# Kernel optimization log

Measured on AMD Instinct MI355X. Metric: run time of the kernel, lower is better.

## Reference

```python
import jax, jax.numpy as jnp
import numpy as np
from jax import lax

B, D, N, K, POOL = 256, 512, 50000, 32, 1024
ALPHA, BETA, LAMB = 1.0, 1.0, 1e-4
TAU, EPS, DELTA = 0.1, 0.1, 1e-3
SINKHORN_ITERS = 200


def matrix_sqrt(A):
    # differentiable symmetric PSD matrix sqrt via eigendecomposition
    w, v = jnp.linalg.eigh(A)
    w = jnp.clip(w, 0.0)
    return (v * jnp.sqrt(w)) @ v.T


def ridge_cov(M, delta):
    Dm = M.shape[0]
    S = M + (jnp.trace(M) / Dm * delta) * jnp.eye(Dm, dtype=M.dtype)
    return 0.5 * (S + S.T)


def sinkhorn(p, q, C, eps):
    # entropic OT, fixed-iteration Sinkhorn (ot.sinkhorn equivalent)
    Kmat = jnp.exp(-C / eps)
    def step(uv, _):
        u, v = uv
        u = p / (Kmat @ v + 1e-16)
        v = q / (Kmat.T @ u + 1e-16)
        return (u, v), None
    (u, v), _ = lax.scan(step, (jnp.ones_like(p), jnp.ones_like(q)), None, length=SINKHORN_ITERS)
    return u[:, None] * Kmat * v[None, :]


def setup_inputs():
    key = jax.random.key(0)
    k1, k2, k3, k4, k5, k6 = jax.random.split(key, 6)
    return {
        "q_batch": jax.random.normal(k1, (B, D), jnp.float32),
        "q_indices": jax.random.randint(k2, (B,), 0, POOL),
        "W": jax.random.normal(k3, (D, D), jnp.float32) * 0.05,
        "X": jax.random.normal(k4, (N, D), jnp.float32),
        "pre_indices": jax.random.randint(k5, (POOL, K), 0, N),
        "pre_weights": jax.random.uniform(k6, (POOL, K), jnp.float32, 0.1, 1.0),
    }


def _forward(q_batch, W, X, pre_weights, q_indices, pre_indices):
    T = q_batch @ W  # model := single linear layer, T_q_batch [B, D]
    # ---- distribution alignment (2-Wasserstein between Gaussians) ----
    mu_X = X.mean(0)
    Sigma_X = ridge_cov(jnp.cov(X, rowvar=False).astype(X.dtype), DELTA)
    mu_t = T.mean(0)
    Sigma_t = ridge_cov(jnp.cov(T, rowvar=False).astype(T.dtype), max(DELTA, 1e-4))
    term_mean = jnp.sum((mu_t - mu_X) ** 2)
    s_t = matrix_sqrt(Sigma_t)
    M = s_t @ Sigma_X @ s_t
    s_m = matrix_sqrt(0.5 * (M + M.T))
    term_cov = jnp.trace(Sigma_X + Sigma_t - 2.0 * s_m)
    loss_dist = term_mean + jnp.clip(term_cov, 0.0)
    # ---- kNN consistency with entropic OT ----
    T_sg = lax.stop_gradient(T)  # faiss search is on detached queries
    d2 = (T_sg ** 2).sum(1, keepdims=True) - 2.0 * T_sg @ X.T + (X ** 2).sum(1)[None, :]
    _, post_idx = lax.top_k(-d2, K)  # exact brute-force kNN == faiss IndexFlatL2
    Xn = X[post_idx]  # [B, K, D]
    l2 = ((T[:, None, :] - Xn) ** 2).sum(-1)  # [B, K], grads flow through T
    post_w = jax.nn.softmax(-l2 / TAU, axis=1)
    post_w = jnp.clip(post_w, 1e-8)
    post_w = post_w / post_w.sum(1, keepdims=True)
    pre_idx_b = pre_indices[q_indices]  # [B, K]
    pre_w = jnp.clip(pre_weights[q_indices], 1e-8)
    pre_w = pre_w / pre_w.sum(1, keepdims=True)
    # fixed-size support = concat(pre, post) of size 2K; duplicated points cost 0
    # to move between, so OT value matches the deduped-union formulation
    support = jnp.concatenate([pre_idx_b, post_idx], axis=1)  # [B, 2K]
    S = X[support]  # [B, 2K, D]
    sq = (S ** 2).sum(-1)
    C = jnp.clip(sq[:, :, None] + sq[:, None, :] - 2.0 * jnp.einsum('bid,bjd->bij', S, S), 0.0)
    med = jnp.median(C.reshape(C.shape[0], -1), axis=1)
    C = C / (med[:, None, None] + 1e-8)
    zeros = jnp.zeros_like(pre_w)
    p = jnp.concatenate([pre_w, zeros], axis=1)   # pre mass on first K slots
    q = jnp.concatenate([zeros, post_w], axis=1)  # post mass on last K slots
    plans = jax.vmap(lambda pp, qq, cc: sinkhorn(pp, qq, cc, EPS))(p, q, C)
    loss_knn = (plans * C).sum((1, 2)).mean()
    loss_reg = 0.5 * jnp.sum(W ** 2)
    total = ALPHA * loss_dist + BETA * loss_knn + LAMB * loss_reg
    return total, loss_dist, loss_knn


def reference(q_batch, q_indices, W, X, pre_indices, pre_weights):
    return _forward(q_batch, W, X, pre_weights, q_indices, pre_indices)
```

## Files before the change

kernel.cpp:

```cpp
#include <hip/hip_runtime.h>
#include <float.h>
#include <math.h>

#define BB 256
#define DD 512
#define NN 50000
#define KK 32
#define NS_ITERS 11
#define PARTS 8
#define PCH 6250

#define OFF_G     0
#define OFF_SC    262144
#define OFF_CS    262208
#define OFF_CSS   262720
#define ZERO_F    263232
#define OFF_T     263232
#define OFF_TC    394304
#define OFF_P     525376
#define OFF_H     656448
#define OFF_XSQ   723008
#define OFF_RUNI  781200
#define OFF_PW    789392
#define OFF_PRW   797584
// ... 151 lines not shown
  }
  for (int kc = 0; kc < 512; kc += 64) {
#pragma unroll
    for (int f = 0; f < 8; ++f) {
      int sa = (f * 16 + r_) * 72 + c4_;
      cvt_write(pa[f], Ah, Al, sa);
      cvt_write(pb[f], Bh, Bl, sa);
    }
    __syncthreads();
    if (kc < 448) {
      int kn = kc + 64;
#pragma unroll
      for (int f = 0; f < 8; ++f) {
        int r = f * 16 + r_;
        pa[f] = *(const float4*)&T[(bi * 128 + r) * 512 + kn + c4_];
        int jg = bj * 128 + r;
        float4 vb = {0.f, 0.f, 0.f, 0.f};
        if (jg < NN) vb = *(const float4*)&X[(size_t)jg * 512 + kn + c4_];
        pb[f] = vb;
      }
    }
#pragma unroll
    for (int ks = 0; ks < 2; ++ks) {
      int kb = ks * 32 + lq * 8;
      bf16x8 ah[4], al[4], bh[4], bl[4];
#pragma unroll
      for (int mi = 0; mi < 4; ++mi) {
        int ro = (m0 + mi * 16 + lrow) * 72 + kb;
        ah[mi] = *(const bf16x8*)&Ah[ro];
        al[mi] = *(const bf16x8*)&Al[ro];
      }
#pragma unroll
      for (int nj = 0; nj < 4; ++nj) {
        int ro = (n0 + nj * 16 + lrow) * 72 + kb;
        bh[nj] = *(const bf16x8*)&Bh[ro];
        bl[nj] = *(const bf16x8*)&Bl[ro];
      }
#pragma unroll
      for (int mi = 0; mi < 4; ++mi)
#pragma unroll
        for (int nj = 0; nj < 4; ++nj) {
          acc[mi][nj] = __builtin_amdgcn_mfma_f32_16x16x32_bf16(ah[mi], bh[nj], acc[mi][nj], 0, 0, 0);
          acc[mi][nj] = __builtin_amdgcn_mfma_f32_16x16x32_bf16(ah[mi], bl[nj], acc[mi][nj], 0, 0, 0);
          acc[mi][nj] = __builtin_amdgcn_mfma_f32_16x16x32_bf16(al[mi], bh[nj], acc[mi][nj], 0, 0, 0);
        }
    }
    __syncthreads();
  }
  if (t < 128) colpart[t] = 0.f;
  __syncthreads();
#pragma unroll
  for (int mi = 0; mi < 4; ++mi)
#pragma unroll
    for (int nj = 0; nj < 4; ++nj)
#pragma unroll
      for (int r = 0; r < 4; ++r) {
        int row = bi * 128 + m0 + mi * 16 + lq * 4 + r;
        int col = bj * 128 + n0 + nj * 16 + lrow;
        if (col < NN) V[(size_t)row * NN + col] = acc[mi][nj][r];
      }
#pragma unroll
  for (int nj = 0; nj < 4; ++nj) {
    float s = 0.f;
#pragma unroll
    for (int mi = 0; mi < 4; ++mi)
#pragma unroll
      for (int r = 0; r < 4; ++r) s += acc[mi][nj][r];
    atomicAdd(&colpart[n0 + nj * 16 + lrow], s);
  }
  __syncthreads();
  if (t < 128) {
    int col = bj * 128 + t;
    if (col < NN) atomicAdd(&m[col], colpart[t] * (1.0f / 256.0f));
  }
}

__global__ void __launch_bounds__(256) k_uut(const float* __restrict__ V,
                                             const float* __restrict__ m,
                                             float* __restrict__ UUT) {
  __shared__ unsigned short Ah[128 * 72], Al[128 * 72], Bh[128 * 72], Bl[128 * 72];
  __shared__ __align__(16) float ms[1000];
  const int pi_[3] = {0, 0, 1}, pj_[3] = {0, 1, 1};
  int bi = pi_[blockIdx.x], bj = pj_[blockIdx.x];
  int j0 = blockIdx.y * 1000, jlim = j0 + 1000;
  int t = threadIdx.x;
  int wave = t >> 6, lane = t & 63;
  int m0 = (wave >> 1) * 64, n0 = (wave & 1) * 64;
  int lrow = lane & 15, lq = lane >> 4;
  int r_ = t >> 4, c4_ = (t & 15) * 4;
  f32x4 acc[4][4] = {};
  if (t < 250) ((float4*)ms)[t] = *(const float4*)&m[j0 + t * 4];
  float4 pa[8], pb[8];
#pragma unroll
  for (int f = 0; f < 8; ++f) {
    int r = f * 16 + r_;
    int jb = j0 + c4_;
    float4 va = {0.f, 0.f, 0.f, 0.f}, vb = {0.f, 0.f, 0.f, 0.f};
    if (jb < jlim) {
      va = *(const float4*)&V[(size_t)(bi * 128 + r) * NN + jb];
      vb = *(const float4*)&V[(size_t)(bj * 128 + r) * NN + jb];
    }
    pa[f] = va; pb[f] = vb;
  }
  __syncthreads();
  for (int ch = 0; ch < 16; ++ch) {
    int jc = j0 + ch * 64;
#pragma unroll
    for (int f = 0; f < 8; ++f) {
      int sa = (f * 16 + r_) * 72 + c4_;
      int jb = jc + c4_;
      float4 va = pa[f], vb = pb[f];
      if (jb < jlim) {
        float4 mm = *(const float4*)&ms[jb - j0];
        va.x -= mm.x; va.y -= mm.y; va.z -= mm.z; va.w -= mm.w;
        vb.x -= mm.x; vb.y -= mm.y; vb.z -= mm.z; vb.w -= mm.w;
      }
      cvt_write(va, Ah, Al, sa);
      cvt_write(vb, Bh, Bl, sa);
    }
    __syncthreads();
    if (ch < 15) {
      int jn = j0 + (ch + 1) * 64;
#pragma unroll
      for (int f = 0; f < 8; ++f) {
        int r = f * 16 + r_;
        int jb = jn + c4_;
        float4 va = {0.f, 0.f, 0.f, 0.f}, vb = {0.f, 0.f, 0.f, 0.f};
        if (jb < jlim) {
          va = *(const float4*)&V[(size_t)(bi * 128 + r) * NN + jb];
          vb = *(const float4*)&V[(size_t)(bj * 128 + r) * NN + jb];
        }
        pa[f] = va; pb[f] = vb;
      }
    }
#pragma unroll
    for (int ks = 0; ks < 2; ++ks) {
      int kb = ks * 32 + lq * 8;
      bf16x8 ah[4], al[4], bh[4], bl[4];
#pragma unroll
      for (int mi = 0; mi < 4; ++mi) {
        int ro = (m0 + mi * 16 + lrow) * 72 + kb;
        ah[mi] = *(const bf16x8*)&Ah[ro];
        al[mi] = *(const bf16x8*)&Al[ro];
      }
#pragma unroll
      for (int nj = 0; nj < 4; ++nj) {
        int ro = (n0 + nj * 16 + lrow) * 72 + kb;
        bh[nj] = *(const bf16x8*)&Bh[ro];
        bl[nj] = *(const bf16x8*)&Bl[ro];
      }
#pragma unroll
      for (int mi = 0; mi < 4; ++mi)
#pragma unroll
        for (int nj = 0; nj < 4; ++nj) {
          acc[mi][nj] = __builtin_amdgcn_mfma_f32_16x16x32_bf16(ah[mi], bh[nj], acc[mi][nj], 0, 0, 0);
          acc[mi][nj] = __builtin_amdgcn_mfma_f32_16x16x32_bf16(ah[mi], bl[nj], acc[mi][nj], 0, 0, 0);
          acc[mi][nj] = __builtin_amdgcn_mfma_f32_16x16x32_bf16(al[mi], bh[nj], acc[mi][nj], 0, 0, 0);
        }
    }
    __syncthreads();
  }
#pragma unroll
  for (int mi = 0; mi < 4; ++mi)
#pragma unroll
    for (int nj = 0; nj < 4; ++nj)
#pragma unroll
      for (int r = 0; r < 4; ++r) {
        int row = bi * 128 + m0 + mi * 16 + lq * 4 + r;
        int col = bj * 128 + n0 + nj * 16 + lrow;
        atomicAdd(&UUT[row * 256 + col], acc[mi][nj][r]);
      }
}

__global__ void __launch_bounds__(256) k_colstatX(const float* __restrict__ X, float* __restrict__ colsum,
                                                  float* __restrict__ colss, float* __restrict__ xsq) {
  __shared__ float shs[512], shq[512];
  int b = blockIdx.x, t = threadIdx.x;
  int wave = t >> 6, lane = t & 63;
  shs[t] = 0.f; shq[t] = 0.f; shs[t + 256] = 0.f; shq[t + 256] = 0.f;
  __syncthreads();
  int c0 = lane * 4;
  float s0 = 0, s1 = 0, s2 = 0, s3 = 0, s4 = 0, s5 = 0, s6 = 0, s7 = 0;
  float q0 = 0, q1 = 0, q2 = 0, q3 = 0, q4 = 0, q5 = 0, q6 = 0, q7 = 0;
  int r0 = b * 200 + wave * 50;
  for (int rr = 0; rr < 50; ++rr) {
    const float* Xr = X + (size_t)(r0 + rr) * 512;
    float4 a = *(const float4*)&Xr[c0];
    float4 c = *(const float4*)&Xr[c0 + 256];
    s0 += a.x; s1 += a.y; s2 += a.z; s3 += a.w;
    s4 += c.x; s5 += c.y; s6 += c.z; s7 += c.w;
    float ax = a.x * a.x, ay = a.y * a.y, az = a.z * a.z, aw = a.w * a.w;
    float cx = c.x * c.x, cy = c.y * c.y, cz = c.z * c.z, cw = c.w * c.w;
    q0 += ax; q1 += ay; q2 += az; q3 += aw;
    q4 += cx; q5 += cy; q6 += cz; q7 += cw;
    float rsq = waveSum(((ax + ay) + (az + aw)) + ((cx + cy) + (cz + cw)));
    if (lane == 0) xsq[r0 + rr] = rsq;
  }
  atomicAdd(&shs[c0 + 0], s0); atomicAdd(&shs[c0 + 1], s1);
  atomicAdd(&shs[c0 + 2], s2); atomicAdd(&shs[c0 + 3], s3);
  atomicAdd(&shs[c0 + 256], s4); atomicAdd(&shs[c0 + 257], s5);
  atomicAdd(&shs[c0 + 258], s6); atomicAdd(&shs[c0 + 259], s7);
  atomicAdd(&shq[c0 + 0], q0); atomicAdd(&shq[c0 + 1], q1);
  atomicAdd(&shq[c0 + 2], q2); atomicAdd(&shq[c0 + 3], q3);
  atomicAdd(&shq[c0 + 256], q4); atomicAdd(&shq[c0 + 257], q5);
  atomicAdd(&shq[c0 + 258], q6); atomicAdd(&shq[c0 + 259], q7);
  __syncthreads();
  atomicAdd(&colsum[t], shs[t]);             atomicAdd(&colss[t], shq[t]);
  atomicAdd(&colsum[t + 256], shs[t + 256]); atomicAdd(&colss[t + 256], shq[t + 256]);
}

__global__ void k_centerT(const float* __restrict__ T, const float* __restrict__ mu,
                          float* __restrict__ Tc, float* __restrict__ scal) {
  __shared__ float red[4];
  int t = threadIdx.x;
  int base = blockIdx.x * 1024;
  float ss = 0.f;
#pragma unroll
  for (int p = 0; p < 4; ++p) {
    int l = base + p * 256 + t;
    float v = T[l] - mu[l & 511] * (1.0f / 256.0f);
    Tc[l] = v;
    ss += v * v;
  }
  ss = waveSum(ss);
  if ((t & 63) == 0) red[t >> 6] = ss;
  __syncthreads();
  if (t == 0) atomicAdd(&scal[0], red[0] + red[1] + red[2] + red[3]);
}

__global__ void k_trCX(const float* __restrict__ colsum, const float* __restrict__ colss,
                       float* __restrict__ scal) {
  __shared__ float red[8];
// ... 7 lines not shown
    float s = 0;
    for (int i = 0; i < 8; ++i) s += red[i];
    scal[1] = s;
  }
}

__global__ void __launch_bounds__(256) k_wvec(const float* __restrict__ T,
                                              const float* __restrict__ colsum,
                                              float* __restrict__ w, float* __restrict__ scal) {
  __shared__ float cs[512];
  int t = threadIdx.x, lane = t & 63, wv_ = t >> 6;
  cs[t] = colsum[t] * (1.0f / 50000.0f);
  cs[t + 256] = colsum[t + 256] * (1.0f / 50000.0f);
  __syncthreads();
  int rbase = blockIdx.x * 32 + wv_ * 8;
  float tot = 0.f;
  for (int rr = 0; rr < 8; ++rr) {
    int row = rbase + rr;
    float a = 0.f;
#pragma unroll
    for (int d = 0; d < 8; ++d) a += T[row * 512 + lane + 64 * d] * cs[lane + 64 * d];
    a = waveSum(a);
    if (lane == 0) { w[row] = a; tot += a; }
  }
  if (lane == 0) atomicAdd(&scal[6], tot);
}

__global__ void k_hfix(const float* __restrict__ UUT, const float* __restrict__ TcTc,
                       const float* __restrict__ w, const float* __restrict__ scal,
                       float* __restrict__ H) {
  int l = blockIdx.x * 256 + threadIdx.x;
  int i = l >> 8, j = l & 255;
  float u = (i >= 128 && j < 128) ? UUT[j * 256 + i] : UUT[i * 256 + j];
  float rho = scal[1] * (1e-3f / 512.0f);
  float wm = scal[6] * (1.0f / 256.0f);
  float wi = w[i] - wm, wj = w[j] - wm;
  H[l] = (u - 50000.0f * wi * wj) * (1.0f / (49999.0f * 255.0f))
       + rho * TcTc[i * 256 + j] * (1.0f / 255.0f);
}

__global__ void __launch_bounds__(256) k_power(const float* __restrict__ H,
                                               float* __restrict__ scal) {
  __shared__ float v[256], nv[256], red[4];
  int t = threadIdx.x;
  float rt = scal[0] * (1.0f / 255.0f) * (1e-3f / 512.0f);
  v[t] = 1.0f;
  __syncthreads();
  float n2 = 256.0f, n3 = 256.0f;
  for (int it = 0; it < 3; ++it) {
    float s = rt * v[t];
    for (int j = 0; j < 256; ++j) s += H[j * 256 + t] * v[j];
    nv[t] = s;
    float ss = waveSum(s * s);
    if ((t & 63) == 0) red[t >> 6] = ss;
    __syncthreads();
    float norm2 = red[0] + red[1] + red[2] + red[3];
    if (it == 1) n2 = norm2;
    if (it == 2) n3 = norm2;
    v[t] = nv[t];
    __syncthreads();
  }
  float d = H[t * 256 + t] + rt;
#pragma unroll
  for (int off = 32; off > 0; off >>= 1) d = fmaxf(d, __shfl_xor(d, off));
  if ((t & 63) == 0) red[t >> 6] = d;
  __syncthreads();
  if (t == 0) {
    float lam = sqrtf(n3 / n2);
    float md = fmaxf(fmaxf(red[0], red[1]), fmaxf(red[2], red[3]));
    scal[5] = fmaxf(1.3f * lam, md);
  }
}

__global__ void k_nsinit(const float* __restrict__ H, const float* __restrict__ scal,
                         float* __restrict__ Y, float* __restrict__ Z) {
  int l = blockIdx.x * 256 + threadIdx.x;
  int i = l >> 8, j = l & 255;
  float rt = scal[0] * (1.0f / 255.0f) * (1e-3f / 512.0f);
  float inv = 1.0f / scal[5];
  Y[l] = (H[l] + ((i == j) ? rt : 0.f)) * inv;
  Z[l] = (i == j) ? 1.0f : 0.f;
}

__global__ void __launch_bounds__(256) k_nsp(const float* __restrict__ Z,
                                             const float* __restrict__ Y,
                                             float* __restrict__ P) {
  __shared__ unsigned short Ah[64 * 72], Al[64 * 72], Bh[64 * 72], Bl[64 * 72];
  int n0b = blockIdx.x * 64, m0b = blockIdx.y * 64;
  int t = threadIdx.x, wave = t >> 6, lane = t & 63;
  int m0 = (wave >> 1) * 32, n0 = (wave & 1) * 32;
  int lrow = lane & 15, lq = lane >> 4;
  f32x4 acc[2][2] = {};
  for (int k0 = 0; k0 < 256; k0 += 64) {
#pragma unroll
    for (int f = 0; f < 4; ++f) {
      int lin = f * 256 + t;
      int r = lin >> 4, c4 = (lin & 15) * 4;
      float4 va = *(const float4*)&Z[(m0b + r) * 256 + k0 + c4];
      cvt_write(va, Ah, Al, r * 72 + c4);
      float4 vb = *(const float4*)&Y[(k0 + r) * 256 + n0b + c4];
      cvt1(vb.x, &Bh[(c4 + 0) * 72 + r], &Bl[(c4 + 0) * 72 + r]);
      cvt1(vb.y, &Bh[(c4 + 1) * 72 + r], &Bl[(c4 + 1) * 72 + r]);
      cvt1(vb.z, &Bh[(c4 + 2) * 72 + r], &Bl[(c4 + 2) * 72 + r]);
      cvt1(vb.w, &Bh[(c4 + 3) * 72 + r], &Bl[(c4 + 3) * 72 + r]);
    }
    __syncthreads();
#pragma unroll
    for (int ks = 0; ks < 2; ++ks) {
      int kb = ks * 32 + lq * 8;
      bf16x8 ah[2], al2[2], bh[2], bl2[2];
#pragma unroll
      for (int mi = 0; mi < 2; ++mi) {
        int ro = (m0 + mi * 16 + lrow) * 72 + kb;
        ah[mi] = *(const bf16x8*)&Ah[ro];
        al2[mi] = *(const bf16x8*)&Al[ro];
      }
#pragma unroll
      for (int nj = 0; nj < 2; ++nj) {
        int ro = (n0 + nj * 16 + lrow) * 72 + kb;
        bh[nj] = *(const bf16x8*)&Bh[ro];
        bl2[nj] = *(const bf16x8*)&Bl[ro];
      }
#pragma unroll
      for (int mi = 0; mi < 2; ++mi)
#pragma unroll
        for (int nj = 0; nj < 2; ++nj) {
          acc[mi][nj] = __builtin_amdgcn_mfma_f32_16x16x32_bf16(ah[mi], bh[nj], acc[mi][nj], 0, 0, 0);
          acc[mi][nj] = __builtin_amdgcn_mfma_f32_16x16x32_bf16(ah[mi], bl2[nj], acc[mi][nj], 0, 0, 0);
          acc[mi][nj] = __builtin_amdgcn_mfma_f32_16x16x32_bf16(al2[mi], bh[nj], acc[mi][nj], 0, 0, 0);
        }
    }
    __syncthreads();
  }
#pragma unroll
  for (int mi = 0; mi < 2; ++mi)
#pragma unroll
    for (int nj = 0; nj < 2; ++nj)
#pragma unroll
      for (int r = 0; r < 4; ++r) {
        int row = m0b + m0 + mi * 16 + lq * 4 + r;
        int col = n0b + n0 + nj * 16 + lrow;
        P[row * 256 + col] = acc[mi][nj][r];
      }
}

__global__ void __launch_bounds__(256) k_nsu(const float* __restrict__ Y, const float* __restrict__ Z,
                                             const float* __restrict__ Pm,
                                             float* __restrict__ Yn, float* __restrict__ Zn) {
  __shared__ unsigned short Ah[64 * 72], Al[64 * 72], Bh[64 * 72], Bl[64 * 72];
  int zz = blockIdx.z;
  const float* A = zz ? Pm : Y;
  const float* B = zz ? Z : Pm;
  const float* D = zz ? Z : Y;
  float* O = zz ? Zn : Yn;
  int n0b = blockIdx.x * 64, m0b = blockIdx.y * 64;
  int t = threadIdx.x, wave = t >> 6, lane = t & 63;
  int m0 = (wave >> 1) * 32, n0 = (wave & 1) * 32;
  int lrow = lane & 15, lq = lane >> 4;
  f32x4 acc[2][2] = {};
  for (int k0 = 0; k0 < 256; k0 += 64) {
#pragma unroll
    for (int f = 0; f < 4; ++f) {
      int lin = f * 256 + t;
      int r = lin >> 4, c4 = (lin & 15) * 4;
      float4 va = *(const float4*)&A[(m0b + r) * 256 + k0 + c4];
      cvt_write(va, Ah, Al, r * 72 + c4);
      float4 vb = *(const float4*)&B[(k0 + r) * 256 + n0b + c4];
      cvt1(vb.x, &Bh[(c4 + 0) * 72 + r], &Bl[(c4 + 0) * 72 + r]);
      cvt1(vb.y, &Bh[(c4 + 1) * 72 + r], &Bl[(c4 + 1) * 72 + r]);
      cvt1(vb.z, &Bh[(c4 + 2) * 72 + r], &Bl[(c4 + 2) * 72 + r]);
      cvt1(vb.w, &Bh[(c4 + 3) * 72 + r], &Bl[(c4 + 3) * 72 + r]);
    }
    __syncthreads();
#pragma unroll
    for (int ks = 0; ks < 2; ++ks) {
      int kb = ks * 32 + lq * 8;
      bf16x8 ah[2], al2[2], bh[2], bl2[2];
#pragma unroll
      for (int mi = 0; mi < 2; ++mi) {
        int ro = (m0 + mi * 16 + lrow) * 72 + kb;
        ah[mi] = *(const bf16x8*)&Ah[ro];
        al2[mi] = *(const bf16x8*)&Al[ro];
      }
#pragma unroll
      for (int nj = 0; nj < 2; ++nj) {
        int ro = (n0 + nj * 16 + lrow) * 72 + kb;
        bh[nj] = *(const bf16x8*)&Bh[ro];
        bl2[nj] = *(const bf16x8*)&Bl[ro];
      }
#pragma unroll
      for (int mi = 0; mi < 2; ++mi)
#pragma unroll
        for (int nj = 0; nj < 2; ++nj) {
          acc[mi][nj] = __builtin_amdgcn_mfma_f32_16x16x32_bf16(ah[mi], bh[nj], acc[mi][nj], 0, 0, 0);
          acc[mi][nj] = __builtin_amdgcn_mfma_f32_16x16x32_bf16(ah[mi], bl2[nj], acc[mi][nj], 0, 0, 0);
          acc[mi][nj] = __builtin_amdgcn_mfma_f32_16x16x32_bf16(al2[mi], bh[nj], acc[mi][nj], 0, 0, 0);
        }
    }
    __syncthreads();
  }
#pragma unroll
  for (int mi = 0; mi < 2; ++mi)
#pragma unroll
    for (int nj = 0; nj < 2; ++nj)
#pragma unroll
      for (int r = 0; r < 4; ++r) {
        int row = m0b + m0 + mi * 16 + lq * 4 + r;
        int col = n0b + n0 + nj * 16 + lrow;
        int idx = row * 256 + col;
        O[idx] = 1.5f * D[idx] - 0.5f * acc[mi][nj][r];
      }
}

__global__ void k_ns_trace(const float* __restrict__ Y, float* __restrict__ scal) {
  __shared__ float red[4];
  int t = threadIdx.x;
  float v = Y[t * 256 + t];
  v = waveSum(v);
  if ((t & 63) == 0) red[t >> 6] = v;
  __syncthreads();
  if (t == 0) {
    float tr = red[0] + red[1] + red[2] + red[3];
    float rt = scal[0] * (1.0f / 255.0f) * (1e-3f / 512.0f);
    scal[2] = sqrtf(scal[5]) * tr + 256.0f * sqrtf(rt);
  }
}

__global__ void __launch_bounds__(256) k_topk_part(const float* __restrict__ V,
                                                   const float* __restrict__ xsq,
                                                   float* __restrict__ candv,
                                                   int* __restrict__ candi) {
  __shared__ float bufv[512];
  __shared__ int bufi[512];
  __shared__ int lcount;
  __shared__ float tvs;
  __shared__ int tis;
  int part = blockIdx.x, q = blockIdx.y, t = threadIdx.x;
  int base = part * PCH;
  int lane = t & 63;
  if (t == 0) { lcount = 0; tvs = FLT_MAX; tis = 0x7fffffff; }
  __syncthreads();
  const float* rowV = V + (size_t)q * NN + base;
  const float* xs = xsq + base;

  auto flush = [&]() {
    __syncthreads();
    int c = lcount;
    for (int s = c + t; s < 512; s += 256) { bufv[s] = FLT_MAX; bufi[s] = 0x7fffffff; }
    __syncthreads();
    for (int ssz = 2; ssz <= 512; ssz <<= 1) {
      for (int st = ssz >> 1; st > 0; st >>= 1) {
        int i = 2 * t - (t & (st - 1));
        int j = i + st;
        bool up = ((i & ssz) == 0);
        float a = bufv[i], b = bufv[j];
        int ai = bufi[i], bi2 = bufi[j];
        bool agtb = (a > b) || (a == b && ai > bi2);
        if (agtb == up) { bufv[i] = b; bufv[j] = a; bufi[i] = bi2; bufi[j] = ai; }
        __syncthreads();
      }
    }
    if (t == 0) { lcount = 32; tvs = bufv[31]; tis = bufi[31]; }
    __syncthreads();
  };

  int ntile = (PCH + 255) >> 8;
  for (int tile = 0; tile < ntile; ++tile) {
    int j = tile * 256 + t;
    float val = 0.f; int idx = 0;
    bool pred = false;
    if (j < PCH) {
      val = xs[j] - 2.0f * rowV[j];
      idx = base + j;
      float tv = tvs; int ti = tis;
      pred = (val < tv) || (val == tv && idx < ti);
    }
    unsigned long long mask = __ballot(pred);
    if (mask) {
      int lead = __ffsll((unsigned long long)mask) - 1;
      int cnt = __popcll(mask);
      int basep = 0;
      if (lane == lead) basep = atomicAdd(&lcount, cnt);
      basep = __shfl(basep, lead);
      if (pred) {
        int off = __popcll(mask & ((1ull << lane) - 1ull));
        int slot = basep + off;
        bufv[slot] = val; bufi[slot] = idx;
      }
    }
    __syncthreads();
    if (lcount >= 256) flush();
  }
  flush();
  if (t < 32) {
    candv[(q * PARTS + part) * 32 + t] = bufv[t];
    candi[(q * PARTS + part) * 32 + t] = bufi[t];
  }
}

__global__ void __launch_bounds__(128) k_topk_final(const float* __restrict__ candv,
                                                    const int* __restrict__ candi,
                                                    int* __restrict__ runi) {
  __shared__ float v[256];
  __shared__ int ix[256];
  int q = blockIdx.x, t = threadIdx.x;
  v[t] = candv[q * 256 + t];
  v[t + 128] = candv[q * 256 + t + 128];
  ix[t] = candi[q * 256 + t];
  ix[t + 128] = candi[q * 256 + t + 128];
  __syncthreads();
  for (int ssz = 2; ssz <= 256; ssz <<= 1) {
    for (int st = ssz >> 1; st > 0; st >>= 1) {
      int i = 2 * t - (t & (st - 1));
      int j = i + st;
      bool up = ((i & ssz) == 0);
      float a = v[i], b = v[j];
      int ai = ix[i], bi = ix[j];
      bool agtb = (a > b) || (a == b && ai > bi);
      if (agtb == up) { v[i] = b; v[j] = a; ix[i] = bi; ix[j] = ai; }
      __syncthreads();
    }
  }
  if (t < 32) runi[q * 32 + t] = ix[t];
}

__global__ void __launch_bounds__(256) k_l2soft(const float* __restrict__ T, const float* __restrict__ X,
                                                const int* __restrict__ runi, const int* __restrict__ qidx,
                                                const float* __restrict__ prew, float* __restrict__ postw,
                                                float* __restrict__ prewn) {
  __shared__ float l2s[32];
  int b = blockIdx.x, t = threadIdx.x;
  int wave = t >> 6, lane = t & 63;
  int qi = qidx[b];
  if (wave == 0) {
    float pwv = (lane < 32) ? fmaxf(prew[qi * 32 + lane], 1e-8f) : 0.f;
    float psum = waveSum(pwv);
    if (lane < 32) prewn[b * 32 + lane] = pwv / psum;
  }
  const float* Tb = T + b * 512;
#pragma unroll
  for (int n8 = 0; n8 < 8; ++n8) {
    int n = wave * 8 + n8;
    int nb = runi[b * 32 + n];
    const float* Xr = X + (size_t)nb * 512;
    float acc = 0.f;
#pragma unroll
    for (int d = 0; d < 8; ++d) {
      float df = Tb[lane + 64 * d] - Xr[lane + 64 * d];
      acc += df * df;
    }
    acc = waveSum(acc);
    if (lane == 0) l2s[n] = acc;
  }
  __syncthreads();
  if (wave == 0) {
    float lg = (lane < 32) ? (-l2s[lane] * 10.0f) : -FLT_MAX;
    float mx = lg;
#pragma unroll
    for (int off = 32; off > 0; off >>= 1) mx = fmaxf(mx, __shfl_xor(mx, off));
    float e = (lane < 32) ? expf(lg - mx) : 0.f;
    float es = waveSum(e);
    float wv = e / es;
    wv = fmaxf(wv, 1e-8f);
    float ws2 = (lane < 32) ? wv : 0.f;
    ws2 = waveSum(ws2);
    if (lane < 32) postw[b * 32 + lane] = wv / ws2;
  }
}

__global__ void __launch_bounds__(256) k_batch(const float* __restrict__ X, const int* __restrict__ qidx,
                                               const int* __restrict__ pre_idx, const int* __restrict__ runi,
                                               const float* __restrict__ prewn, const float* __restrict__ postw,
                                               float* __restrict__ scal) {
  __shared__ float G[64][65];
  __shared__ float Cm[64][65];
  __shared__ unsigned short Ah[64 * 72], Al[64 * 72];
  __shared__ int supp[64];
  __shared__ float uuS[32], vvS[32];
  __shared__ float red[4];
  __shared__ float medsh;
  __shared__ unsigned int cw[4], mw[4];
  int b = blockIdx.x, t = threadIdx.x;
  int wave = t >> 6, lane = t & 63;
  if (t < 32) supp[t] = pre_idx[qidx[b] * 32 + t];
  else if (t < 64) supp[t] = runi[b * 32 + t - 32];
  __syncthreads();
  {
    int m0 = (wave >> 1) * 32, n0 = (wave & 1) * 32;
    int lrow = lane & 15, lq = lane >> 4;
    int r_ = t >> 4, c4_ = (t & 15) * 4;
    f32x4 acc[2][2] = {};
    float4 pf[4];
#pragma unroll
    for (int f = 0; f < 4; ++f) {
      int r = f * 16 + r_;
      pf[f] = *(const float4*)&X[(size_t)supp[r] * 512 + c4_];
    }
    for (int kc = 0; kc < 512; kc += 64) {
#pragma unroll
      for (int f = 0; f < 4; ++f)
        cvt_write(pf[f], Ah, Al, (f * 16 + r_) * 72 + c4_);
      __syncthreads();
      if (kc < 448) {
        int kn = kc + 64;
#pragma unroll
        for (int f = 0; f < 4; ++f) {
          int r = f * 16 + r_;
          pf[f] = *(const float4*)&X[(size_t)supp[r] * 512 + kn + c4_];
        }
      }
#pragma unroll
      for (int ks = 0; ks < 2; ++ks) {
        int kb = ks * 32 + lq * 8;
        bf16x8 ah[2], al[2], bh[2], bl[2];
#pragma unroll
        for (int mi = 0; mi < 2; ++mi) {
          int ro = (m0 + mi * 16 + lrow) * 72 + kb;
          ah[mi] = *(const bf16x8*)&Ah[ro];
          al[mi] = *(const bf16x8*)&Al[ro];
        }
#pragma unroll
        for (int nj = 0; nj < 2; ++nj) {
          int ro = (n0 + nj * 16 + lrow) * 72 + kb;
          bh[nj] = *(const bf16x8*)&Ah[ro];
          bl[nj] = *(const bf16x8*)&Al[ro];
        }
#pragma unroll
        for (int mi = 0; mi < 2; ++mi)
#pragma unroll
          for (int nj = 0; nj < 2; ++nj) {
            acc[mi][nj] = __builtin_amdgcn_mfma_f32_16x16x32_bf16(ah[mi], bh[nj], acc[mi][nj], 0, 0, 0);
            acc[mi][nj] = __builtin_amdgcn_mfma_f32_16x16x32_bf16(ah[mi], bl[nj], acc[mi][nj], 0, 0, 0);
            acc[mi][nj] = __builtin_amdgcn_mfma_f32_16x16x32_bf16(al[mi], bh[nj], acc[mi][nj], 0, 0, 0);
          }
      }
      __syncthreads();
    }
#pragma unroll
    for (int mi = 0; mi < 2; ++mi)
#pragma unroll
      for (int nj = 0; nj < 2; ++nj)
#pragma unroll
        for (int r = 0; r < 4; ++r)
          G[m0 + mi * 16 + lq * 4 + r][n0 + nj * 16 + lrow] = acc[mi][nj][r];
  }
  __syncthreads();
  unsigned int uval[16];
#pragma unroll
  for (int s = 0; s < 16; ++s) {
    int l = s * 256 + t;
    int i = l >> 6, j = l & 63;
    float cc = fmaxf(G[i][i] + G[j][j] - 2.0f * G[i][j], 0.f);
    Cm[i][j] = cc;
    uval[s] = (i < j) ? (__float_as_uint(cc) & 0x7fffffffu) : 0xffffffffu;
  }
  unsigned int ans = 0;
  for (int bb = 30; bb >= 0; --bb) {
    unsigned int test = ans | (1u << bb);
    int cw_ = 0;
#pragma unroll
    for (int s = 0; s < 16; ++s)
      cw_ += __popcll(__ballot(uval[s] < test));
    __syncthreads();
    if (lane == 0) red[wave] = (float)cw_;
    __syncthreads();
    int cnt = (int)(red[0] + red[1] + red[2] + red[3]);
    if (cnt < 992) ans = test;
  }
  {
    unsigned int target = ans;
    unsigned int cnt = 0, mn = 0xffffffffu;
#pragma unroll
    for (int s = 0; s < 16; ++s) {
      unsigned int u = uval[s];
      if (u <= target) cnt++;
      else mn = (u < mn) ? u : mn;
    }
#pragma unroll
    for (int off = 32; off > 0; off >>= 1) {
      cnt += __shfl_xor(cnt, off);
      unsigned int m2 = __shfl_xor(mn, off);
      mn = (m2 < mn) ? m2 : mn;
    }
    __syncthreads();
    if (lane == 0) { cw[wave] = cnt; mw[wave] = mn; }
    __syncthreads();
    if (t == 0) {
      unsigned int ct = cw[0] + cw[1] + cw[2] + cw[3];
      unsigned int mt = mw[0];
      mt = (mw[1] < mt) ? mw[1] : mt;
      mt = (mw[2] < mt) ? mw[2] : mt;
      mt = (mw[3] < mt) ? mw[3] : mt;
      float v992 = __uint_as_float(target);
      float v993 = (ct >= 993u) ? v992 : __uint_as_float(mt);
      medsh = 0.5f * (v992 + v993) + 1e-8f;
    }
    __syncthreads();
  }
  float inv = 1.0f / medsh;
  for (int l = t; l < 4096; l += 256) {
    int i = l >> 6, j = l & 63;
    float cn = Cm[i][j] * inv;
    Cm[i][j] = cn;
    G[i][j] = expf(-cn * 10.0f);
  }
  __syncthreads();
  if (wave == 0) {
    int half = lane >> 5;
    int l = lane & 31;
    int cb = half * 16;
    float p_l = prewn[b * 32 + l];
    float q_l = postw[b * 32 + l];
    float Kr16[16], Kt16[16];
#pragma unroll
    for (int c2 = 0; c2 < 16; ++c2) Kr16[c2] = G[l][32 + cb + c2];
#pragma unroll
    for (int r2 = 0; r2 < 16; ++r2) Kt16[r2] = G[cb + r2][32 + l];
    float r0 = 0.f;
#pragma unroll
    for (int c2 = 0; c2 < 32; ++c2) r0 += G[l][half * 32 + c2];
    r0 += __shfl_xor(r0, 32);
    float u = p_l / (r0 + 1e-16f);
    float s0 = 0.f, s1 = 0.f, s2 = 0.f, s3 = 0.f;
#pragma unroll
    for (int r2 = 0; r2 < 16; r2 += 4) {
      s0 += Kt16[r2]     * __shfl(u, cb + r2);
      s1 += Kt16[r2 + 1] * __shfl(u, cb + r2 + 1);
      s2 += Kt16[r2 + 2] * __shfl(u, cb + r2 + 2);
      s3 += Kt16[r2 + 3] * __shfl(u, cb + r2 + 3);
    }
    float sv = (s0 + s1) + (s2 + s3);
    sv += __shfl_xor(sv, 32);
    float v = q_l / (sv + 1e-16f);
    float pu = u, pv = v;
    float ppu = 0.f, ppv = 0.f;
    for (int it = 1; it < 200; ++it) {
      float a0 = 0.f, a1 = 0.f, a2 = 0.f, a3 = 0.f;
#pragma unroll
      for (int c2 = 0; c2 < 16; c2 += 4) {
        a0 += Kr16[c2]     * __shfl(v, cb + c2);
        a1 += Kr16[c2 + 1] * __shfl(v, cb + c2 + 1);
        a2 += Kr16[c2 + 2] * __shfl(v, cb + c2 + 2);
        a3 += Kr16[c2 + 3] * __shfl(v, cb + c2 + 3);
      }
      float au = (a0 + a1) + (a2 + a3);
      au += __shfl_xor(au, 32);
      u = p_l / (au + 1e-16f);
      a0 = 0.f; a1 = 0.f; a2 = 0.f; a3 = 0.f;
#pragma unroll
      for (int r2 = 0; r2 < 16; r2 += 4) {
        a0 += Kt16[r2]     * __shfl(u, cb + r2);
        a1 += Kt16[r2 + 1] * __shfl(u, cb + r2 + 1);
        a2 += Kt16[r2 + 2] * __shfl(u, cb + r2 + 2);
        a3 += Kt16[r2 + 3] * __shfl(u, cb + r2 + 3);
      }
      float bv = (a0 + a1) + (a2 + a3);
      bv += __shfl_xor(bv, 32);
      v = q_l / (bv + 1e-16f);
      if (__all(u == pu && v == pv)) break;
      if (it >= 2 && __all(u == ppu && v == ppv)) {
        if ((199 - it) & 1) { u = pu; v = pv; }
        break;
      }
      ppu = pu; ppv = pv; pu = u; pv = v;
    }
    if (t < 32) { uuS[t] = u; vvS[t] = v; }
  }
  __syncthreads();
  float lacc = 0.f;
#pragma unroll
  for (int q8 = 0; q8 < 4; ++q8) {
    int l = q8 * 256 + t;
    int i = l >> 5, j = l & 31;
    lacc += uuS[i] * G[i][32 + j] * vvS[j] * Cm[i][32 + j];
  }
  lacc = waveSum(lacc);
  if ((t & 63) == 0) red[t >> 6] = lacc;
  __syncthreads();
  if (t == 0)
    atomicAdd(&scal[3], (red[0] + red[1] + red[2] + red[3]) * (1.0f / 256.0f));
}

__global__ void k_wreg(const float* __restrict__ W, float* __restrict__ scal) {
  __shared__ float red[4];
  int t = threadIdx.x;
  int base = blockIdx.x * 2048;
  float ss = 0.f;
#pragma unroll
  for (int p = 0; p < 8; ++p) {
    float v = W[base + p * 256 + t];
    ss += v * v;
  }
  ss = waveSum(ss);
  if ((t & 63) == 0) red[t >> 6] = ss;
  __syncthreads();
  if (t == 0) atomicAdd(&scal[4], red[0] + red[1] + red[2] + red[3]);
}

__global__ void k_combine(const float* __restrict__ mu_t, const float* __restrict__ colsum,
                          const float* __restrict__ scal, float* __restrict__ out) {
  __shared__ float red[8];
  int t = threadIdx.x;
  float dm = mu_t[t] * (1.0f / 256.0f) - colsum[t] * (1.0f / 50000.0f);
  float v = dm * dm;
  v = waveSum(v);
  if ((t & 63) == 0) red[t >> 6] = v;
  __syncthreads();
  if (t == 0) {
    float term_mean = 0.f;
    for (int i = 0; i < 8; ++i) term_mean += red[i];
    float trCT = scal[0] * (1.0f / 255.0f);
    float trCX = scal[1];
    float S = scal[2];
    float term_cov = trCX * 1.001f + trCT * 1.001f - 2.0f * S;
    term_cov = fmaxf(term_cov, 0.f);
    float loss_dist = term_mean + term_cov;
    float loss_knn = scal[3];
    float loss_reg = 0.5f * scal[4];
    out[0] = loss_dist + loss_knn + 1e-4f * loss_reg;
    out[1] = loss_dist;
    out[2] = loss_knn;
  }
}

extern "C" void kernel_launch(void* const* d_in, const int* in_sizes, int n_in,
                              void* d_out, int out_size, void* d_ws, size_t ws_size,
                              hipStream_t stream) {
  const float* q = (const float*)d_in[0];
  const int* qidx = (const int*)d_in[1];
  const float* W = (const float*)d_in[2];
  const float* X = (const float*)d_in[3];
  const int* pre_idx = (const int*)d_in[4];
  const float* prew = (const float*)d_in[5];
  float* out = (float*)d_out;
  float* ws = (float*)d_ws;

  float* scal = ws + OFF_SC;
  float* colsum = ws + OFF_CS;
  float* colss = ws + OFF_CSS;
  float* T = ws + OFF_T;
  float* Tc = ws + OFF_TC;
  float* H = ws + OFF_H;
  float* mu_t = ws + OFF_MUT;
  float* xsq = ws + OFF_XSQ;
  int* runi = (int*)(ws + OFF_RUNI);
  float* postw = ws + OFF_PW;
  float* prewn = ws + OFF_PRW;
  float* V = ws + OFF_D2;
  float* UUT = ws + OFF_UUT;
  float* TcTc = ws + OFF_TCTC;
  float* wv = ws + OFF_W;
  float* m = ws + OFF_M;
  float* candv = ws + OFF_P;
  int* candi = (int*)(ws + OFF_P + 65536);

  hipMemsetAsync(d_ws, 0, (size_t)ZERO_F * 4, stream);

  k_g64_nn<<<dim3(8, 4), 256, 0, stream>>>(q, W, T, 512, 512, 512, 512, 1.0f, mu_t);
  k_colstatX<<<250, 256, 0, stream>>>(X, colsum, colss, xsq);
  k_centerT<<<128, 256, 0, stream>>>(T, mu_t, Tc, scal);
  k_trCX<<<1, 512, 0, stream>>>(colsum, colss, scal);
  k_vgemm<<<dim3(391, 2), 256, 0, stream>>>(T, X, V, m);
  k_topk_part<<<dim3(PARTS, 256), 256, 0, stream>>>(V, xsq, candv, candi);
  k_topk_final<<<256, 128, 0, stream>>>(candv, candi, runi);
  k_g64_nt<<<dim3(4, 4), 256, 0, stream>>>(Tc, Tc, TcTc, 512, 512, 512, 256, 1.0f);
  k_wvec<<<8, 256, 0, stream>>>(T, colsum, wv, scal);
  k_uut<<<dim3(3, 50), 256, 0, stream>>>(V, m, UUT);
  k_hfix<<<256, 256, 0, stream>>>(UUT, TcTc, wv, scal, H);
  {
    float* Y = ws + OFF_TC;
    float* Z = ws + OFF_TC + 65536;
    float* Y2 = ws + OFF_P;
    float* Z2 = ws + OFF_P + 65536;
    float* Pm = ws + OFF_G;
    k_power<<<1, 256, 0, stream>>>(H, scal);
    k_nsinit<<<256, 256, 0, stream>>>(H, scal, Y, Z);
    for (int it = 0; it < NS_ITERS; ++it) {
      k_nsp<<<dim3(4, 4), 256, 0, stream>>>(Z, Y, Pm);
      k_nsu<<<dim3(4, 4, 2), 256, 0, stream>>>(Y, Z, Pm, Y2, Z2);
      float* tmp = Y; Y = Y2; Y2 = tmp;
      tmp = Z; Z = Z2; Z2 = tmp;
    }
    k_ns_trace<<<1, 256, 0, stream>>>(Y, scal);
  }
  k_l2soft<<<256, 256, 0, stream>>>(T, X, runi, qidx, prew, postw, prewn);
  k_batch<<<256, 256, 0, stream>>>(X, qidx, pre_idx, runi, prewn, postw, scal);
  k_wreg<<<128, 256, 0, stream>>>(W, scal);
  k_combine<<<1, 512, 0, stream>>>(mu_t, colsum, scal, out);
}
```

Before: 905.3 us.

## Skip redundant loads on diagonal UUT tiles, trim last NS step, single-wave median

Diagonal blocks of the UUT Gram kernel now reuse the A tile as the B operand instead of loading and converting the same rows twice. The final Newton-Schulz iteration only computes the diagonal blocks of the Y update and reduces the trace directly, which removes the Z update and the separate trace kernel. The per-batch median search in k_batch now runs in a single wave over the upper triangle, dropping the block-wide syncs on each bisection step. The NS trace moves to a new scal slot that k_combine reads, which relies on scal[7] lying in the zeroed region, and the median work is serialized onto one wave.

New measurement: 959.7 us. +6.0%, slower.

```diff
diff --git a/kernel.cpp b/kernel.cpp
--- a/kernel.cpp
+++ b/kernel.cpp
@@ -257,6 +257,7 @@
   __shared__ __align__(16) float ms[1000];
   const int pi_[3] = {0, 0, 1}, pj_[3] = {0, 1, 1};
   int bi = pi_[blockIdx.x], bj = pj_[blockIdx.x];
+  bool diag = (bi == bj);
   int j0 = blockIdx.y * 1000, jlim = j0 + 1000;
   int t = threadIdx.x;
   int wave = t >> 6, lane = t & 63;
@@ -273,11 +274,13 @@
     float4 va = {0.f, 0.f, 0.f, 0.f}, vb = {0.f, 0.f, 0.f, 0.f};
     if (jb < jlim) {
       va = *(const float4*)&V[(size_t)(bi * 128 + r) * NN + jb];
-      vb = *(const float4*)&V[(size_t)(bj * 128 + r) * NN + jb];
+      if (!diag) vb = *(const float4*)&V[(size_t)(bj * 128 + r) * NN + jb];
     }
     pa[f] = va; pb[f] = vb;
   }
   __syncthreads();
+  const unsigned short* BhP = diag ? (const unsigned short*)Ah : (const unsigned short*)Bh;
+  const unsigned short* BlP = diag ? (const unsigned short*)Al : (const unsigned short*)Bl;
   for (int ch = 0; ch < 16; ++ch) {
     int jc = j0 + ch * 64;
 #pragma unroll
@@ -288,10 +291,10 @@
       if (jb < jlim) {
         float4 mm = *(const float4*)&ms[jb - j0];
         va.x -= mm.x; va.y -= mm.y; va.z -= mm.z; va.w -= mm.w;
-        vb.x -= mm.x; vb.y -= mm.y; vb.z -= mm.z; vb.w -= mm.w;
+        if (!diag) { vb.x -= mm.x; vb.y -= mm.y; vb.z -= mm.z; vb.w -= mm.w; }
       }
       cvt_write(va, Ah, Al, sa);
-      cvt_write(vb, Bh, Bl, sa);
+      if (!diag) cvt_write(vb, Bh, Bl, sa);
     }
     __syncthreads();
     if (ch < 15) {
@@ -303,7 +306,7 @@
         float4 va = {0.f, 0.f, 0.f, 0.f}, vb = {0.f, 0.f, 0.f, 0.f};
         if (jb < jlim) {
           va = *(const float4*)&V[(size_t)(bi * 128 + r) * NN + jb];
-          vb = *(const float4*)&V[(size_t)(bj * 128 + r) * NN + jb];
+          if (!diag) vb = *(const float4*)&V[(size_t)(bj * 128 + r) * NN + jb];
         }
         pa[f] = va; pb[f] = vb;
       }
@@ -321,8 +324,8 @@
 #pragma unroll
       for (int nj = 0; nj < 4; ++nj) {
         int ro = (n0 + nj * 16 + lrow) * 72 + kb;
-        bh[nj] = *(const bf16x8*)&Bh[ro];
-        bl[nj] = *(const bf16x8*)&Bl[ro];
+        bh[nj] = *(const bf16x8*)&BhP[ro];
+        bl[nj] = *(const bf16x8*)&BlP[ro];
       }
 #pragma unroll
       for (int mi = 0; mi < 4; ++mi)
@@ -496,78 +499,11 @@
   Z[l] = (i == j) ? 1.0f : 0.f;
 }
 
-__global__ void __launch_bounds__(256) k_nsp(const float* __restrict__ Z,
-                                             const float* __restrict__ Y,
-                                             float* __restrict__ P) {
-  __shared__ unsigned short Ah[64 * 72], Al[64 * 72], Bh[64 * 72], Bl[64 * 72];
-  int n0b = blockIdx.x * 64, m0b = blockIdx.y * 64;
-  int t = threadIdx.x, wave = t >> 6, lane = t & 63;
-  int m0 = (wave >> 1) * 32, n0 = (wave & 1) * 32;
-  int lrow = lane & 15, lq = lane >> 4;
-  f32x4 acc[2][2] = {};
-  for (int k0 = 0; k0 < 256; k0 += 64) {
-#pragma unroll
-    for (int f = 0; f < 4; ++f) {
-      int lin = f * 256 + t;
-      int r = lin >> 4, c4 = (lin & 15) * 4;
-      float4 va = *(const float4*)&Z[(m0b + r) * 256 + k0 + c4];
-      cvt_write(va, Ah, Al, r * 72 + c4);
-      float4 vb = *(const float4*)&Y[(k0 + r) * 256 + n0b + c4];
-      cvt1(vb.x, &Bh[(c4 + 0) * 72 + r], &Bl[(c4 + 0) * 72 + r]);
-      cvt1(vb.y, &Bh[(c4 + 1) * 72 + r], &Bl[(c4 + 1) * 72 + r]);
-      cvt1(vb.z, &Bh[(c4 + 2) * 72 + r], &Bl[(c4 + 2) * 72 + r]);
-      cvt1(vb.w, &Bh[(c4 + 3) * 72 + r], &Bl[(c4 + 3) * 72 + r]);
-    }
-    __syncthreads();
-#pragma unroll
-    for (int ks = 0; ks < 2; ++ks) {
-      int kb = ks * 32 + lq * 8;
-      bf16x8 ah[2], al2[2], bh[2], bl2[2];
-#pragma unroll
-      for (int mi = 0; mi < 2; ++mi) {
-        int ro = (m0 + mi * 16 + lrow) * 72 + kb;
-        ah[mi] = *(const bf16x8*)&Ah[ro];
-        al2[mi] = *(const bf16x8*)&Al[ro];
-      }
-#pragma unroll
-      for (int nj = 0; nj < 2; ++nj) {
-        int ro = (n0 + nj * 16 + lrow) * 72 + kb;
-        bh[nj] = *(const bf16x8*)&Bh[ro];
-        bl2[nj] = *(const bf16x8*)&Bl[ro];
-      }
-#pragma unroll
-      for (int mi = 0; mi < 2; ++mi)
-#pragma unroll
-        for (int nj = 0; nj < 2; ++nj) {
-          acc[mi][nj] = __builtin_amdgcn_mfma_f32_16x16x32_bf16(ah[mi], bh[nj], acc[mi][nj], 0, 0, 0);
-          acc[mi][nj] = __builtin_amdgcn_mfma_f32_16x16x32_bf16(ah[mi], bl2[nj], acc[mi][nj], 0, 0, 0);
-          acc[mi][nj] = __builtin_amdgcn_mfma_f32_16x16x32_bf16(al2[mi], bh[nj], acc[mi][nj], 0, 0, 0);
-        }
-    }
-    __syncthreads();
-  }
-#pragma unroll
-  for (int mi = 0; mi < 2; ++mi)
-#pragma unroll
-    for (int nj = 0; nj < 2; ++nj)
-#pragma unroll
-      for (int r = 0; r < 4; ++r) {
-        int row = m0b + m0 + mi * 16 + lq * 4 + r;
-        int col = n0b + n0 + nj * 16 + lrow;
-        P[row * 256 + col] = acc[mi][nj][r];
-      }
-}
-
-__global__ void __launch_bounds__(256) k_nsu(const float* __restrict__ Y, const float* __restrict__ Z,
-                                             const float* __restrict__ Pm,
-                                             float* __restrict__ Yn, float* __restrict__ Zn) {
-  __shared__ unsigned short Ah[64 * 72], Al[64 * 72], Bh[64 * 72], Bl[64 * 72];
-  int zz = blockIdx.z;
-  const float* A = zz ? Pm : Y;
-  const float* B = zz ? Z : Pm;
-  const float* D = zz ? Z : Y;
-  float* O = zz ? Zn : Yn;
-  int n0b = blockIdx.x * 64, m0b = blockIdx.y * 64;
+__device__ __forceinline__ void ns_mfma_tile(const float* __restrict__ A, const float* __restrict__ B,
+                                             const float* __restrict__ D, float* __restrict__ O,
+                                             int m0b, int n0b, float dscale, float ascale,
+                                             unsigned short* Ah, unsigned short* Al,
+                                             unsigned short* Bh, unsigned short* Bl) {
   int t = threadIdx.x, wave = t >> 6, lane = t & 63;
   int m0 = (wave >> 1) * 32, n0 = (wave & 1) * 32;
   int lrow = lane & 15, lq = lane >> 4;
@@ -622,22 +558,97 @@
         int row = m0b + m0 + mi * 16 + lq * 4 + r;
         int col = n0b + n0 + nj * 16 + lrow;
         int idx = row * 256 + col;
-        O[idx] = 1.5f * D[idx] - 0.5f * acc[mi][nj][r];
-      }
-}
-
-__global__ void k_ns_trace(const float* __restrict__ Y, float* __restrict__ scal) {
+        float base = (dscale != 0.f) ? dscale * D[idx] : 0.f;
+        O[idx] = base + ascale * acc[mi][nj][r];
+      }
+}
+
+__global__ void __launch_bounds__(256) k_nsp(const float* __restrict__ Z,
+                                             const float* __restrict__ Y,
+                                             float* __restrict__ P) {
+  __shared__ unsigned short Ah[64 * 72], Al[64 * 72], Bh[64 * 72], Bl[64 * 72];
+  ns_mfma_tile(Z, Y, Z, P, blockIdx.y * 64, blockIdx.x * 64, 0.f, 1.0f, Ah, Al, Bh, Bl);
+}
+
+__global__ void __launch_bounds__(256) k_nsu(const float* __restrict__ Y, const float* __restrict__ Z,
+                                             const float* __restrict__ Pm,
+                                             float* __restrict__ Yn, float* __restrict__ Zn) {
+  __shared__ unsigned short Ah[64 * 72], Al[64 * 72], Bh[64 * 72], Bl[64 * 72];
+  int zz = blockIdx.z;
+  if (zz == 0)
+    ns_mfma_tile(Y, Pm, Y, Yn, blockIdx.y * 64, blockIdx.x * 64, 1.5f, -0.5f, Ah, Al, Bh, Bl);
+  else
+    ns_mfma_tile(Pm, Z, Z, Zn, blockIdx.y * 64, blockIdx.x * 64, 1.5f, -0.5f, Ah, Al, Bh, Bl);
+}
+
+__global__ void __launch_bounds__(256) k_nsu_diag(const float* __restrict__ Y,
+                                                  const float* __restrict__ Pm,
+                                                  float* __restrict__ scal) {
+  __shared__ unsigned short Ah[64 * 72], Al[64 * 72], Bh[64 * 72], Bl[64 * 72];
   __shared__ float red[4];
-  int t = threadIdx.x;
-  float v = Y[t * 256 + t];
-  v = waveSum(v);
-  if ((t & 63) == 0) red[t >> 6] = v;
-  __syncthreads();
-  if (t == 0) {
-    float tr = red[0] + red[1] + red[2] + red[3];
-    float rt = scal[0] * (1.0f / 255.0f) * (1e-3f / 512.0f);
-    scal[2] = sqrtf(scal[5]) * tr + 256.0f * sqrtf(rt);
-  }
+  int bi = blockIdx.x;
+  int m0b = bi * 64, n0b = bi * 64;
+  int t = threadIdx.x, wave = t >> 6, lane = t & 63;
+  int m0 = (wave >> 1) * 32, n0 = (wave & 1) * 32;
+  int lrow = lane & 15, lq = lane >> 4;
+  f32x4 acc[2][2] = {};
+  for (int k0 = 0; k0 < 256; k0 += 64) {
+#pragma unroll
+    for (int f = 0; f < 4; ++f) {
+      int lin = f * 256 + t;
+      int r = lin >> 4, c4 = (lin & 15) * 4;
+      float4 va = *(const float4*)&Y[(m0b + r) * 256 + k0 + c4];
+      cvt_write(va, Ah, Al, r * 72 + c4);
+      float4 vb = *(const float4*)&Pm[(k0 + r) * 256 + n0b + c4];
+      cvt1(vb.x, &Bh[(c4 + 0) * 72 + r], &Bl[(c4 + 0) * 72 + r]);
+      cvt1(vb.y, &Bh[(c4 + 1) * 72 + r], &Bl[(c4 + 1) * 72 + r]);
+      cvt1(vb.z, &Bh[(c4 + 2) * 72 + r], &Bl[(c4 + 2) * 72 + r]);
+      cvt1(vb.w, &Bh[(c4 + 3) * 72 + r], &Bl[(c4 + 3) * 72 + r]);
+    }
+    __syncthreads();
+#pragma unroll
+    for (int ks = 0; ks < 2; ++ks) {
+      int kb = ks * 32 + lq * 8;
+      bf16x8 ah[2], al2[2], bh[2], bl2[2];
+#pragma unroll
+      for (int mi = 0; mi < 2; ++mi) {
+        int ro = (m0 + mi * 16 + lrow) * 72 + kb;
+        ah[mi] = *(const bf16x8*)&Ah[ro];
+        al2[mi] = *(const bf16x8*)&Al[ro];
+      }
+#pragma unroll
+      for (int nj = 0; nj < 2; ++nj) {
+        int ro = (n0 + nj * 16 + lrow) * 72 + kb;
+        bh[nj] = *(const bf16x8*)&Bh[ro];
+        bl2[nj] = *(const bf16x8*)&Bl[ro];
+      }
+#pragma unroll
+      for (int mi = 0; mi < 2; ++mi)
+#pragma unroll
+        for (int nj = 0; nj < 2; ++nj) {
+          acc[mi][nj] = __builtin_amdgcn_mfma_f32_16x16x32_bf16(ah[mi], bh[nj], acc[mi][nj], 0, 0, 0);
+          acc[mi][nj] = __builtin_amdgcn_mfma_f32_16x16x32_bf16(ah[mi], bl2[nj], acc[mi][nj], 0, 0, 0);
+          acc[mi][nj] = __builtin_amdgcn_mfma_f32_16x16x32_bf16(al2[mi], bh[nj], acc[mi][nj], 0, 0, 0);
+        }
+    }
+    __syncthreads();
+  }
+  float lacc = 0.f;
+#pragma unroll
+  for (int mi = 0; mi < 2; ++mi)
+#pragma unroll
+    for (int nj = 0; nj < 2; ++nj)
+#pragma unroll
+      for (int r = 0; r < 4; ++r) {
+        int row = m0 + mi * 16 + lq * 4 + r;
+        int col = n0 + nj * 16 + lrow;
+        if (row == col)
+          lacc += 1.5f * Y[(m0b + row) * 256 + n0b + col] - 0.5f * acc[mi][nj][r];
+      }
+  lacc = waveSum(lacc);
+  if ((t & 63) == 0) red[t >> 6] = lacc;
+  __syncthreads();
+  if (t == 0) atomicAdd(&scal[7], red[0] + red[1] + red[2] + red[3]);
 }
 
 __global__ void __launch_bounds__(256) k_topk_part(const float* __restrict__ V,
@@ -793,7 +804,6 @@
   __shared__ float uuS[32], vvS[32];
   __shared__ float red[4];
   __shared__ float medsh;
-  __shared__ unsigned int cw[4], mw[4];
   int b = blockIdx.x, t = threadIdx.x;
   int wave = t >> 6, lane = t & 63;
   if (t < 32) supp[t] = pre_idx[qidx[b] * 32 + t];
@@ -859,58 +869,45 @@
           G[m0 + mi * 16 + lq * 4 + r][n0 + nj * 16 + lrow] = acc[mi][nj][r];
   }
   __syncthreads();
-  unsigned int uval[16];
-#pragma unroll
-  for (int s = 0; s < 16; ++s) {
-    int l = s * 256 + t;
+  for (int l = t; l < 4096; l += 256) {
     int i = l >> 6, j = l & 63;
-    float cc = fmaxf(G[i][i] + G[j][j] - 2.0f * G[i][j], 0.f);
-    Cm[i][j] = cc;
-    uval[s] = (i < j) ? (__float_as_uint(cc) & 0x7fffffffu) : 0xffffffffu;
-  }
-  unsigned int ans = 0;
-  for (int bb = 30; bb >= 0; --bb) {
-    unsigned int test = ans | (1u << bb);
-    int cw_ = 0;
-#pragma unroll
-    for (int s = 0; s < 16; ++s)
-      cw_ += __popcll(__ballot(uval[s] < test));
-    __syncthreads();
-    if (lane == 0) red[wave] = (float)cw_;
-    __syncthreads();
-    int cnt = (int)(red[0] + red[1] + red[2] + red[3]);
-    if (cnt < 992) ans = test;
-  }
-  {
-    unsigned int target = ans;
-    unsigned int cnt = 0, mn = 0xffffffffu;
-#pragma unroll
-    for (int s = 0; s < 16; ++s) {
-      unsigned int u = uval[s];
-      if (u <= target) cnt++;
-      else mn = (u < mn) ? u : mn;
+    Cm[i][j] = fmaxf(G[i][i] + G[j][j] - 2.0f * G[i][j], 0.f);
+  }
+  __syncthreads();
+  if (wave == 0) {
+    unsigned int uv2[64];
+#pragma unroll
+    for (int s = 0; s < 64; ++s)
+      uv2[s] = (s < lane) ? (__float_as_uint(Cm[s][lane]) & 0x7fffffffu) : 0xffffffffu;
+    unsigned int ans = 0;
+    for (int bb2 = 30; bb2 >= 0; --bb2) {
+      unsigned int test = ans | (1u << bb2);
+      int cnt = 0;
+#pragma unroll
+      for (int s = 0; s < 64; ++s)
+        cnt += __popcll(__ballot(uv2[s] < test));
+      if (cnt < 992) ans = test;
+    }
+    unsigned int cnt2 = 0, mn = 0xffffffffu;
+#pragma unroll
+    for (int s = 0; s < 64; ++s) {
+      unsigned int u2 = uv2[s];
+      if (u2 <= ans) cnt2++;
+      else mn = (u2 < mn) ? u2 : mn;
     }
 #pragma unroll
     for (int off = 32; off > 0; off >>= 1) {
-      cnt += __shfl_xor(cnt, off);
+      cnt2 += __shfl_xor(cnt2, off);
       unsigned int m2 = __shfl_xor(mn, off);
       mn = (m2 < mn) ? m2 : mn;
     }
-    __syncthreads();
-    if (lane == 0) { cw[wave] = cnt; mw[wave] = mn; }
-    __syncthreads();
-    if (t == 0) {
-      unsigned int ct = cw[0] + cw[1] + cw[2] + cw[3];
-      unsigned int mt = mw[0];
-      mt = (mw[1] < mt) ? mw[1] : mt;
-      mt = (mw[2] < mt) ? mw[2] : mt;
-      mt = (mw[3] < mt) ? mw[3] : mt;
-      float v992 = __uint_as_float(target);
-      float v993 = (ct >= 993u) ? v992 : __uint_as_float(mt);
+    if (lane == 0) {
+      float v992 = __uint_as_float(ans);
+      float v993 = (cnt2 >= 993u) ? v992 : __uint_as_float(mn);
       medsh = 0.5f * (v992 + v993) + 1e-8f;
     }
-    __syncthreads();
-  }
+  }
+  __syncthreads();
   float inv = 1.0f / medsh;
   for (int l = t; l < 4096; l += 256) {
     int i = l >> 6, j = l & 63;
@@ -946,7 +943,7 @@
     float sv = (s0 + s1) + (s2 + s3);
     sv += __shfl_xor(sv, 32);
     float v = q_l / (sv + 1e-16f);
-    float pu = u, pv = v;
+    float pu = u, pv2 = v;
     float ppu = 0.f, ppv = 0.f;
     for (int it = 1; it < 200; ++it) {
       float a0 = 0.f, a1 = 0.f, a2 = 0.f, a3 = 0.f;
@@ -971,12 +968,12 @@
       float bv = (a0 + a1) + (a2 + a3);
       bv += __shfl_xor(bv, 32);
       v = q_l / (bv + 1e-16f);
-      if (__all(u == pu && v == pv)) break;
+      if (__all(u == pu && v == pv2)) break;
       if (it >= 2 && __all(u == ppu && v == ppv)) {
-        if ((199 - it) & 1) { u = pu; v = pv; }
+        if ((199 - it) & 1) { u = pu; v = pv2; }
         break;
       }
-      ppu = pu; ppv = pv; pu = u; pv = v;
+      ppu = pu; ppv = pv2; pu = u; pv2 = v;
     }
     if (t < 32) { uuS[t] = u; vvS[t] = v; }
   }
@@ -1025,7 +1022,8 @@
     for (int i = 0; i < 8; ++i) term_mean += red[i];
     float trCT = scal[0] * (1.0f / 255.0f);
     float trCX = scal[1];
-    float S = scal[2];
+    float rt = scal[0] * (1.0f / 255.0f) * (1e-3f / 512.0f);
+    float S = sqrtf(scal[5]) * scal[7] + 256.0f * sqrtf(rt);
     float term_cov = trCX * 1.001f + trCT * 1.001f - 2.0f * S;
     term_cov = fmaxf(term_cov, 0.f);
     float loss_dist = term_mean + term_cov;
@@ -1080,22 +1078,23 @@
   k_g64_nt<<<dim3(4, 4), 256, 0, stream>>>(Tc, Tc, TcTc, 512, 512, 512, 256, 1.0f);
   k_wvec<<<8, 256, 0, stream>>>(T, colsum, wv, scal);
   k_uut<<<dim3(3, 50), 256, 0, stream>>>(V, m, UUT);
-  k_hfix<<<256, 256, 0, stream>>>(UUT, TcTc, wv, scal, H);
   {
     float* Y = ws + OFF_TC;
     float* Z = ws + OFF_TC + 65536;
     float* Y2 = ws + OFF_P;
     float* Z2 = ws + OFF_P + 65536;
     float* Pm = ws + OFF_G;
+    k_hfix<<<256, 256, 0, stream>>>(UUT, TcTc, wv, scal, H);
     k_power<<<1, 256, 0, stream>>>(H, scal);
     k_nsinit<<<256, 256, 0, stream>>>(H, scal, Y, Z);
-    for (int it = 0; it < NS_ITERS; ++it) {
+    for (int it = 0; it < NS_ITERS - 1; ++it) {
       k_nsp<<<dim3(4, 4), 256, 0, stream>>>(Z, Y, Pm);
       k_nsu<<<dim3(4, 4, 2), 256, 0, stream>>>(Y, Z, Pm, Y2, Z2);
       float* tmp = Y; Y = Y2; Y2 = tmp;
       tmp = Z; Z = Z2; Z2 = tmp;
     }
-    k_ns_trace<<<1, 256, 0, stream>>>(Y, scal);
+    k_nsp<<<dim3(4, 4), 256, 0, stream>>>(Z, Y, Pm);
+    k_nsu_diag<<<4, 256, 0, stream>>>(Y, Pm, scal);
   }
   k_l2soft<<<256, 256, 0, stream>>>(T, X, runi, qidx, prew, postw, prewn);
   k_batch<<<256, 256, 0, stream>>>(X, qidx, pre_idx, runi, prewn, postw, scal);
```
